# Optimization experiments

Hardware: AMD Instinct MI355X
Metric: run time of the kernel (lower is better)

The kernel has to match this reference:

```python
import jax, jax.numpy as jnp
import numpy as np

NB, NT, P = 20000, 1000, 50000
MARGIN = 2.0
LAM = 0.5          # lambda_param
TOPK = 5
RANK_W = 0.3
NEG_SENT = -1e9    # sentinel for masked-out (positive-labeled) entries


def setup_inputs() -> dict:
    key = jax.random.key(0)
    k1, k2, k3 = jax.random.split(key, 3)
    scores = jax.random.normal(k1, (NB, NT), dtype=jnp.float32)
    pair_bacteria = jax.random.randint(k2, (P,), 0, NB)
    pair_traits = jax.random.randint(k3, (P,), 0, NT)
    return {"scores": scores, "pair_bacteria": pair_bacteria, "pair_traits": pair_traits}


def reference(scores, pair_bacteria, pair_traits):
    nb, nt = scores.shape
    # scatter labels: labels[b, t] = 1 for each positive pair
    labels = jnp.zeros_like(scores).at[pair_bacteria, pair_traits].set(1.0)

    # HCMGNN-style weighted squared-diff loss on sigmoid predictions
    preds = jax.nn.sigmoid(scores)
    diff = labels - preds
    total = float(nb * nt)
    sq = diff * diff
    positive_loss = jnp.sum(labels * sq) / total
    negative_loss = jnpp_sum = jnp.sum((1.0 - labels) * sq) / total
    loss = (1.0 - LAM) * positive_loss + LAM * negative_loss

    # per-positive-pair top-k margin ranking loss
    rows = scores[pair_bacteria]          # [P, NT]
    row_labels = labels[pair_bacteria]    # [P, NT]
    masked = jnp.where(row_labels == 0.0, rows, NEG_SENT)
    top_neg, _ = jax.lax.top_k(masked, TOPK)               # [P, TOPK]
    pos_score = scores[pair_bacteria, pair_traits]         # [P]
    # sentinel entries give margin - pos + NEG_SENT << 0 -> relu = 0, grad = 0
    contrib = jax.nn.relu(MARGIN - (pos_score[:, None] - top_neg))
    ranking_sum = jnp.sum(contrib)

    num_neg_row = jnp.sum(row_labels == 0.0, axis=1)       # negatives per pair's row
    valid = jnp.minimum(num_neg_row, TOPK)                 # min(5, len(neg_scores))
    num_ranking_pairs = jnp.sum(valid)

    ranking_loss = ranking_sum / jnp.maximum(num_ranking_pairs, 1).astype(scores.dtype)
    loss = jnp.where(num_ranking_pairs > 0, loss + RANK_W * ranking_loss, loss)
    return loss
```

## Files before the change

### kernel.cpp

```cpp
#include <hip/hip_runtime.h>
#include <cstdint>
#include <cstddef>

#define NB 20000
#define NT 1000
#define P_PAIRS 50000
#define MARGIN 2.0f
#define RANK_W 0.3f
#define NEG_SENT -1e9f

#define BLOCK 512
#define ROWS_PB 32
#define NBLOCKS (NB / ROWS_PB)
#define PB4 (P_PAIRS / 4)
#define PLIST_CAP 512
#define MROW_W 33


#define INSERT5(x)                                        \
    {                                                     \
        float _x = (x);                                   \
        float n0 = fmaxf(t0, _x), s0_ = fminf(t0, _x);    \
        float n1 = fmaxf(t1, s0_), s1_ = fminf(t1, s0_);  \
        float n2 = fmaxf(t2, s1_), s2_ = fminf(t2, s1_);  \
        float n3 = fmaxf(t3, s2_), s3_ = fminf(t3, s2_);  \
        float n4 = fmaxf(t4, s3_);                        \
        t0 = n0; t1 = n1; t2 = n2; t3 = n3; t4 = n4;      \
    }

#define PROC1(xv, lab)                                              \
    {                                                               \
        float _x = (xv);                                            \
        int _lab = (lab);                                           \
        float _s = __builtin_amdgcn_rcpf(1.0f + __expf(-_x));       \
        float _d = (float)_lab - _s;                                \
        sq = fmaf(_d, _d, sq);                                      \
        pcount += _lab;                                             \
        float _xx = _lab ? NEG_SENT : _x;                           \
        INSERT5(_xx);                                               \
    }

#define PROC4(v, bits)                        \
    PROC1((v).x, (int)(((bits) >> 0) & 1u));  \
    PROC1((v).y, (int)(((bits) >> 1) & 1u));  \
    PROC1((v).z, (int)(((bits) >> 2) & 1u));  \
    PROC1((v).w, (int)(((bits) >> 3) & 1u));

#define SCAN4(v, idx)                                                   \
    {                                                                   \
        int _bs[4] = {(v).x, (v).y, (v).z, (v).w};                      \
        _Pragma("unroll")                                               \
        for (int _j = 0; _j < 4; ++_j) {                                \
            unsigned int _d = (unsigned int)(_bs[_j] - rowBase);        \
            if (_d < (unsigned int)ROWS_PB) {                           \
                int _t = pt[(idx) * 4 + _j];                            \
                atomicOr(&smask[_d * MROW_W + (_t >> 5)], 1u << (_t & 31)); \
                int _k = atomicAdd(&pcnt, 1);                           \
                if (_k < PLIST_CAP) plist[_k] = ((int)_d << 10) | _t;   \
            }                                                           \
        }                                                               \
    }

__global__ __launch_bounds__(BLOCK)
void fused_row_pair_kernel(const float* __restrict__ scores,
                           const int* __restrict__ pb,
                           const int* __restrict__ pt,
                           float4* __restrict__ partials) {
    const int tid  = threadIdx.x;
    const int lane = tid & 63;
    const int wib  = tid >> 6;
    const int grp  = lane >> 4;
    const int gl   = lane & 15;
    const int rowBase = blockIdx.x * ROWS_PB;

    __shared__ unsigned int smask[ROWS_PB * MROW_W];
    __shared__ float  stop5[ROWS_PB][5];
    __shared__ int    snn[ROWS_PB];
    __shared__ int    plist[PLIST_CAP];
    __shared__ int    pcnt;
    __shared__ float  bsq[ROWS_PB];
    __shared__ float  sc[8];
    __shared__ unsigned int sv[8];

    for (int i = tid; i < ROWS_PB * MROW_W; i += BLOCK) smask[i] = 0u;
    if (tid == 0) pcnt = 0;
    __syncthreads();

    const int4* pb4 = reinterpret_cast<const int4*>(pb);
    #pragma unroll 1
    for (int base = tid; base + 1536 < PB4; base += 2048) {
        int4 va = pb4[base       ];
        int4 vb = pb4[base +  512];
        int4 vc = pb4[base + 1024];
        int4 vd = pb4[base + 1536];
        SCAN4(va, base);
        SCAN4(vb, base +  512);
        SCAN4(vc, base + 1024);
        SCAN4(vd, base + 1536);
    }
    {
        int idx = 12288 + tid;
        if (idx < PB4) {
            int4 v = pb4[idx];
            SCAN4(v, idx);
        }
    }
    __syncthreads();

    const int localRow = wib * 4 + grp;
    const int row = rowBase + localRow;
    const float4* rowp = reinterpret_cast<const float4*>(scores + (size_t)row * NT);
    const unsigned int* mrow = smask + localRow * MROW_W;
    const int wb = gl >> 3;
    const int sh = (gl & 7) * 4;

    float t0 = NEG_SENT, t1 = NEG_SENT, t2 = NEG_SENT, t3 = NEG_SENT, t4 = NEG_SENT;
    float sq = 0.0f;
    int pcount = 0;

    {
        float4 v0  = rowp[gl      ];
        float4 v1  = rowp[gl +  16];
        float4 v2  = rowp[gl +  32];
        float4 v3  = rowp[gl +  48];
        unsigned int b0 = (mrow[wb     ] >> sh) & 0xFu;
        unsigned int b1 = (mrow[wb +  2] >> sh) & 0xFu;
        unsigned int b2 = (mrow[wb +  4] >> sh) & 0xFu;
        unsigned int b3 = (mrow[wb +  6] >> sh) & 0xFu;
        PROC4(v0, b0); PROC4(v1, b1); PROC4(v2, b2); PROC4(v3, b3);
    }
    {
        float4 v0  = rowp[gl +  64];
        float4 v1  = rowp[gl +  80];
        float4 v2  = rowp[gl +  96];
        float4 v3  = rowp[gl + 112];
        unsigned int b0 = (mrow[wb +  8] >> sh) & 0xFu;
        unsigned int b1 = (mrow[wb + 10] >> sh) & 0xFu;
        unsigned int b2 = (mrow[wb + 12] >> sh) & 0xFu;
        unsigned int b3 = (mrow[wb + 14] >> sh) & 0xFu;
        PROC4(v0, b0); PROC4(v1, b1); PROC4(v2, b2); PROC4(v3, b3);
    }
    {
        float4 v0  = rowp[gl + 128];
        float4 v1  = rowp[gl + 144];
        float4 v2  = rowp[gl + 160];
        float4 v3  = rowp[gl + 176];
        unsigned int b0 = (mrow[wb + 16] >> sh) & 0xFu;
        unsigned int b1 = (mrow[wb + 18] >> sh) & 0xFu;
        unsigned int b2 = (mrow[wb + 20] >> sh) & 0xFu;
        unsigned int b3 = (mrow[wb + 22] >> sh) & 0xFu;
        PROC4(v0, b0); PROC4(v1, b1); PROC4(v2, b2); PROC4(v3, b3);
    }
    {
        float4 v0  = rowp[gl + 192];
        float4 v1  = rowp[gl + 208];
        float4 v2  = rowp[gl + 224];
        unsigned int b0 = (mrow[wb + 24] >> sh) & 0xFu;
        unsigned int b1 = (mrow[wb + 26] >> sh) & 0xFu;
        unsigned int b2 = (mrow[wb + 28] >> sh) & 0xFu;
        PROC4(v0, b0); PROC4(v1, b1); PROC4(v2, b2);
    }
    if (gl < 10) {
        float4 v = rowp[gl + 240];
        unsigned int bt = (mrow[wb + 30] >> sh) & 0xFu;
        PROC4(v, bt);
    }

    #pragma unroll
    for (int off = 8; off >= 1; off >>= 1) {
        float b0 = __shfl_xor(t0, off, 16);
        float b1 = __shfl_xor(t1, off, 16);
        float b2 = __shfl_xor(t2, off, 16);
        float b3 = __shfl_xor(t3, off, 16);
        float b4 = __shfl_xor(t4, off, 16);
        sq     += __shfl_xor(sq, off, 16);
        pcount += __shfl_xor(pcount, off, 16);

        float m1  = fminf(t0, b0);
        float m2a = fminf(t1, b0), m2b = fminf(t0, b1);
        float m3a = fminf(t2, b0), m3b = fminf(t1, b1), m3c = fminf(t0, b2);
        float m4a = fminf(t3, b0), m4b = fminf(t2, b1), m4c = fminf(t1, b2), m4d = fminf(t0, b3);
        float c0 = fmaxf(t0, b0);
        float c1 = fmaxf(fmaxf(t1, b1), m1);
        float c2 = fmaxf(fmaxf(t2, b2), fmaxf(m2a, m2b));
        float c3 = fmaxf(fmaxf(t3, b3), fmaxf(fmaxf(m3a, m3b), m3c));
        float c4 = fmaxf(fmaxf(t4, b4), fmaxf(fmaxf(m4a, m4b), fmaxf(m4c, m4d)));
        t0 = c0; t1 = c1; t2 = c2; t3 = c3; t4 = c4;
    }

    if (gl == 0) {
        stop5[localRow][0] = t0; stop5[localRow][1] = t1; stop5[localRow][2] = t2;
        stop5[localRow][3] = t3; stop5[localRow][4] = t4;
        snn[localRow] = NT - pcount;
        bsq[localRow] = sq;
    }
    __syncthreads();

    float c = 0.0f;
    unsigned int valid = 0;
    int np = pcnt;
    if (np <= PLIST_CAP) {
        for (int k = tid; k < np; k += BLOCK) {
            int e = plist[k];
            int lr = e >> 10, t = e & 1023;
            float pos = scores[(size_t)(rowBase + lr) * NT + t];
            #pragma unroll
            for (int q = 0; q < 5; ++q) {
                float contrib = MARGIN - (pos - stop5[lr][q]);
                c += contrib > 0.0f ? contrib : 0.0f;
            }
            int nn = snn[lr];
            valid += (unsigned int)(nn < 5 ? nn : 5);
        }
    } else {
        for (int i = tid; i < PB4; i += BLOCK) {
            int4 v = pb4[i];
            int bs[4] = {v.x, v.y, v.z, v.w};
            #pragma unroll
            for (int j = 0; j < 4; ++j) {
                unsigned int d = (unsigned int)(bs[j] - rowBase);
                if (d < (unsigned int)ROWS_PB) {
                    int t = pt[i * 4 + j];
                    float pos = scores[(size_t)(rowBase + d) * NT + t];
                    #pragma unroll
                    for (int q = 0; q < 5; ++q) {
                        float contrib = MARGIN - (pos - stop5[d][q]);
                        c += contrib > 0.0f ? contrib : 0.0f;
                    }
                    int nn = snn[d];
                    valid += (unsigned int)(nn < 5 ? nn : 5);
                }
            }
        }
    }

    #pragma unroll
    for (int off = 32; off >= 1; off >>= 1) {
        c     += __shfl_xor(c, off);
        valid += __shfl_xor(valid, off);
    }
    if ((tid & 63) == 0) { sc[wib] = c; sv[wib] = valid; }
    __syncthreads();
    if (tid == 0) {
        float s = 0.0f;
        #pragma unroll
        for (int k = 0; k < ROWS_PB; ++k) s += bsq[k];
        float cb = 0.0f;
        float vb = 0.0f;
        #pragma unroll
        for (int w = 0; w < 8; ++w) { cb += sc[w]; vb += (float)sv[w]; }
        partials[blockIdx.x] = make_float4(s, cb, vb, 0.0f);
    }
}

__global__ __launch_bounds__(256)
void finalize_kernel(const float4* __restrict__ partials,
                     float* __restrict__ out) {
    float s = 0.0f, cb = 0.0f, vb = 0.0f;
    for (int i = threadIdx.x; i < NBLOCKS; i += 256) {
        float4 p = partials[i];
        s += p.x; cb += p.y; vb += p.z;
    }
    #pragma unroll
    for (int off = 32; off >= 1; off >>= 1) {
        s  += __shfl_xor(s, off);
        cb += __shfl_xor(cb, off);
        vb += __shfl_xor(vb, off);
    }
    __shared__ float ss[4], scc[4], svv[4];
    int wib = threadIdx.x >> 6;
    if ((threadIdx.x & 63) == 0) { ss[wib] = s; scc[wib] = cb; svv[wib] = vb; }
    __syncthreads();
    if (threadIdx.x == 0) {
        float st = ss[0] + ss[1] + ss[2] + ss[3];
        float ct = scc[0] + scc[1] + scc[2] + scc[3];
        float vt = svv[0] + svv[1] + svv[2] + svv[3];
        float loss = 0.5f * st / 2.0e7f;
        if (vt > 0.0f) loss += RANK_W * ct / vt;
        out[0] = loss;
    }
}

extern "C" void kernel_launch(void* const* d_in, const int* in_sizes, int n_in,
                              void* d_out, int out_size, void* d_ws, size_t ws_size,
                              hipStream_t stream) {
    const float* scores = (const float*)d_in[0];
    const int*   pb     = (const int*)d_in[1];
    const int*   pt     = (const int*)d_in[2];
    float*       out    = (float*)d_out;
    float4*      partials = (float4*)d_ws;

    fused_row_pair_kernel<<<NBLOCKS, BLOCK, 0, stream>>>(scores, pb, pt, partials);
    finalize_kernel<<<1, 256, 0, stream>>>(partials, out);
}
```

Measured before the change: 35.65 us.

## Pre-bucket pairs by row block in a scatter kernel instead of per-block full scans

Adds a scatter kernel that buckets positive pairs by 16-row block in global workspace, so each row block reads only its own pairs rather than scanning all pair indices. Rows per block and block size are halved. The final reduction kernel is replaced by global atomics plus a last-block ticket. This adds a zeroing kernel and a scatter kernel launch, and makes the floating-point summation order nondeterministic.

```diff
diff --git a/kernel.cpp b/kernel.cpp
--- a/kernel.cpp
+++ b/kernel.cpp
@@ -9,13 +9,32 @@
 #define RANK_W 0.3f
 #define NEG_SENT -1e9f
 
-#define BLOCK 512
-#define ROWS_PB 32
+#define BLOCK 256
+#define ROWS_PB 16
 #define NBLOCKS (NB / ROWS_PB)
 #define PB4 (P_PAIRS / 4)
-#define PLIST_CAP 512
+#define BUCKET_CAP 256
 #define MROW_W 33
 
+
+__global__ void zero_ctrl_kernel(unsigned int* __restrict__ ws) {
+    int i = blockIdx.x * blockDim.x + threadIdx.x;
+    if (i < 1254) ws[i] = 0u;
+}
+
+__global__ __launch_bounds__(256)
+void scatter_kernel(const int* __restrict__ pb,
+                    const int* __restrict__ pt,
+                    int* __restrict__ counts,
+                    int* __restrict__ lists) {
+    int p = blockIdx.x * 256 + threadIdx.x;
+    if (p >= P_PAIRS) return;
+    int b = pb[p];
+    int t = pt[p];
+    int blk = b >> 4;
+    int idx = atomicAdd(&counts[blk], 1);
+    if (idx < BUCKET_CAP) lists[blk * BUCKET_CAP + idx] = ((b & 15) << 10) | t;
+}
 
 #define INSERT5(x)                                        \
     {                                                     \
@@ -46,26 +65,17 @@
     PROC1((v).z, (int)(((bits) >> 2) & 1u));  \
     PROC1((v).w, (int)(((bits) >> 3) & 1u));
 
-#define SCAN4(v, idx)                                                   \
-    {                                                                   \
-        int _bs[4] = {(v).x, (v).y, (v).z, (v).w};                      \
-        _Pragma("unroll")                                               \
-        for (int _j = 0; _j < 4; ++_j) {                                \
-            unsigned int _d = (unsigned int)(_bs[_j] - rowBase);        \
-            if (_d < (unsigned int)ROWS_PB) {                           \
-                int _t = pt[(idx) * 4 + _j];                            \
-                atomicOr(&smask[_d * MROW_W + (_t >> 5)], 1u << (_t & 31)); \
-                int _k = atomicAdd(&pcnt, 1);                           \
-                if (_k < PLIST_CAP) plist[_k] = ((int)_d << 10) | _t;   \
-            }                                                           \
-        }                                                               \
-    }
-
 __global__ __launch_bounds__(BLOCK)
 void fused_row_pair_kernel(const float* __restrict__ scores,
                            const int* __restrict__ pb,
                            const int* __restrict__ pt,
-                           float4* __restrict__ partials) {
+                           const int* __restrict__ counts,
+                           const int* __restrict__ lists,
+                           float* __restrict__ sq_total,
+                           float* __restrict__ rsum,
+                           unsigned int* __restrict__ nrp,
+                           unsigned int* __restrict__ ticket,
+                           float* __restrict__ out) {
     const int tid  = threadIdx.x;
     const int lane = tid & 63;
     const int wib  = tid >> 6;
@@ -76,33 +86,36 @@
     __shared__ unsigned int smask[ROWS_PB * MROW_W];
     __shared__ float  stop5[ROWS_PB][5];
     __shared__ int    snn[ROWS_PB];
-    __shared__ int    plist[PLIST_CAP];
-    __shared__ int    pcnt;
+    __shared__ int    plist[BUCKET_CAP];
     __shared__ float  bsq[ROWS_PB];
-    __shared__ float  sc[8];
-    __shared__ unsigned int sv[8];
+    __shared__ float  sc[4];
+    __shared__ unsigned int sv[4];
 
     for (int i = tid; i < ROWS_PB * MROW_W; i += BLOCK) smask[i] = 0u;
-    if (tid == 0) pcnt = 0;
-    __syncthreads();
-
-    const int4* pb4 = reinterpret_cast<const int4*>(pb);
-    #pragma unroll 1
-    for (int base = tid; base + 1536 < PB4; base += 2048) {
-        int4 va = pb4[base       ];
-        int4 vb = pb4[base +  512];
-        int4 vc = pb4[base + 1024];
-        int4 vd = pb4[base + 1536];
-        SCAN4(va, base);
-        SCAN4(vb, base +  512);
-        SCAN4(vc, base + 1024);
-        SCAN4(vd, base + 1536);
-    }
-    {
-        int idx = 12288 + tid;
-        if (idx < PB4) {
-            int4 v = pb4[idx];
-            SCAN4(v, idx);
+    __syncthreads();
+
+    const int rawCnt = counts[blockIdx.x];
+    const bool overflow = rawCnt > BUCKET_CAP;
+    const int cnt = overflow ? 0 : rawCnt;
+    if (tid < cnt) {
+        int e = lists[blockIdx.x * BUCKET_CAP + tid];
+        plist[tid] = e;
+        int lr = e >> 10, t = e & 1023;
+        atomicOr(&smask[lr * MROW_W + (t >> 5)], 1u << (t & 31));
+    }
+    if (overflow) {
+        const int4* pb4 = reinterpret_cast<const int4*>(pb);
+        for (int i = tid; i < PB4; i += BLOCK) {
+            int4 v = pb4[i];
+            int bs[4] = {v.x, v.y, v.z, v.w};
+            #pragma unroll
+            for (int j = 0; j < 4; ++j) {
+                unsigned int d = (unsigned int)(bs[j] - rowBase);
+                if (d < (unsigned int)ROWS_PB) {
+                    int t = pt[i * 4 + j];
+                    atomicOr(&smask[d * MROW_W + (t >> 5)], 1u << (t & 31));
+                }
+            }
         }
     }
     __syncthreads();
@@ -119,10 +132,10 @@
     int pcount = 0;
 
     {
-        float4 v0  = rowp[gl      ];
-        float4 v1  = rowp[gl +  16];
-        float4 v2  = rowp[gl +  32];
-        float4 v3  = rowp[gl +  48];
+        float4 v0 = rowp[gl      ];
+        float4 v1 = rowp[gl +  16];
+        float4 v2 = rowp[gl +  32];
+        float4 v3 = rowp[gl +  48];
         unsigned int b0 = (mrow[wb     ] >> sh) & 0xFu;
         unsigned int b1 = (mrow[wb +  2] >> sh) & 0xFu;
         unsigned int b2 = (mrow[wb +  4] >> sh) & 0xFu;
@@ -130,10 +143,10 @@
         PROC4(v0, b0); PROC4(v1, b1); PROC4(v2, b2); PROC4(v3, b3);
     }
     {
-        float4 v0  = rowp[gl +  64];
-        float4 v1  = rowp[gl +  80];
-        float4 v2  = rowp[gl +  96];
-        float4 v3  = rowp[gl + 112];
+        float4 v0 = rowp[gl +  64];
+        float4 v1 = rowp[gl +  80];
+        float4 v2 = rowp[gl +  96];
+        float4 v3 = rowp[gl + 112];
         unsigned int b0 = (mrow[wb +  8] >> sh) & 0xFu;
         unsigned int b1 = (mrow[wb + 10] >> sh) & 0xFu;
         unsigned int b2 = (mrow[wb + 12] >> sh) & 0xFu;
@@ -141,10 +154,10 @@
         PROC4(v0, b0); PROC4(v1, b1); PROC4(v2, b2); PROC4(v3, b3);
     }
     {
-        float4 v0  = rowp[gl + 128];
-        float4 v1  = rowp[gl + 144];
-        float4 v2  = rowp[gl + 160];
-        float4 v3  = rowp[gl + 176];
+        float4 v0 = rowp[gl + 128];
+        float4 v1 = rowp[gl + 144];
+        float4 v2 = rowp[gl + 160];
+        float4 v3 = rowp[gl + 176];
         unsigned int b0 = (mrow[wb + 16] >> sh) & 0xFu;
         unsigned int b1 = (mrow[wb + 18] >> sh) & 0xFu;
         unsigned int b2 = (mrow[wb + 20] >> sh) & 0xFu;
@@ -152,9 +165,9 @@
         PROC4(v0, b0); PROC4(v1, b1); PROC4(v2, b2); PROC4(v3, b3);
     }
     {
-        float4 v0  = rowp[gl + 192];
-        float4 v1  = rowp[gl + 208];
-        float4 v2  = rowp[gl + 224];
+        float4 v0 = rowp[gl + 192];
+        float4 v1 = rowp[gl + 208];
+        float4 v2 = rowp[gl + 224];
         unsigned int b0 = (mrow[wb + 24] >> sh) & 0xFu;
         unsigned int b1 = (mrow[wb + 26] >> sh) & 0xFu;
         unsigned int b2 = (mrow[wb + 28] >> sh) & 0xFu;
@@ -198,9 +211,8 @@
 
     float c = 0.0f;
     unsigned int valid = 0;
-    int np = pcnt;
-    if (np <= PLIST_CAP) {
-        for (int k = tid; k < np; k += BLOCK) {
+    if (!overflow) {
+        for (int k = tid; k < cnt; k += BLOCK) {
             int e = plist[k];
             int lr = e >> 10, t = e & 1023;
             float pos = scores[(size_t)(rowBase + lr) * NT + t];
@@ -213,6 +225,7 @@
             valid += (unsigned int)(nn < 5 ? nn : 5);
         }
     } else {
+        const int4* pb4 = reinterpret_cast<const int4*>(pb);
         for (int i = tid; i < PB4; i += BLOCK) {
             int4 v = pb4[i];
             int bs[4] = {v.x, v.y, v.z, v.w};
@@ -241,43 +254,24 @@
     }
     if ((tid & 63) == 0) { sc[wib] = c; sv[wib] = valid; }
     __syncthreads();
+
     if (tid == 0) {
         float s = 0.0f;
         #pragma unroll
         for (int k = 0; k < ROWS_PB; ++k) s += bsq[k];
-        float cb = 0.0f;
-        float vb = 0.0f;
-        #pragma unroll
-        for (int w = 0; w < 8; ++w) { cb += sc[w]; vb += (float)sv[w]; }
-        partials[blockIdx.x] = make_float4(s, cb, vb, 0.0f);
-    }
-}
-
-__global__ __launch_bounds__(256)
-void finalize_kernel(const float4* __restrict__ partials,
-                     float* __restrict__ out) {
-    float s = 0.0f, cb = 0.0f, vb = 0.0f;
-    for (int i = threadIdx.x; i < NBLOCKS; i += 256) {
-        float4 p = partials[i];
-        s += p.x; cb += p.y; vb += p.z;
-    }
-    #pragma unroll
-    for (int off = 32; off >= 1; off >>= 1) {
-        s  += __shfl_xor(s, off);
-        cb += __shfl_xor(cb, off);
-        vb += __shfl_xor(vb, off);
-    }
-    __shared__ float ss[4], scc[4], svv[4];
-    int wib = threadIdx.x >> 6;
-    if ((threadIdx.x & 63) == 0) { ss[wib] = s; scc[wib] = cb; svv[wib] = vb; }
-    __syncthreads();
-    if (threadIdx.x == 0) {
-        float st = ss[0] + ss[1] + ss[2] + ss[3];
-        float ct = scc[0] + scc[1] + scc[2] + scc[3];
-        float vt = svv[0] + svv[1] + svv[2] + svv[3];
-        float loss = 0.5f * st / 2.0e7f;
-        if (vt > 0.0f) loss += RANK_W * ct / vt;
-        out[0] = loss;
+        atomicAdd(sq_total, s);
+        atomicAdd(rsum, sc[0] + sc[1] + sc[2] + sc[3]);
+        atomicAdd(nrp,  sv[0] + sv[1] + sv[2] + sv[3]);
+        __threadfence();
+        unsigned int done = atomicAdd(ticket, 1u);
+        if (done == NBLOCKS - 1) {
+            float sqt = atomicAdd(sq_total, 0.0f);
+            float rs  = atomicAdd(rsum, 0.0f);
+            unsigned int n = atomicAdd(nrp, 0u);
+            float loss = 0.5f * sqt / 2.0e7f;
+            if (n > 0) loss += RANK_W * rs / (float)n;
+            out[0] = loss;
+        }
     }
 }
 
@@ -288,8 +282,17 @@
     const int*   pb     = (const int*)d_in[1];
     const int*   pt     = (const int*)d_in[2];
     float*       out    = (float*)d_out;
-    float4*      partials = (float4*)d_ws;
-
-    fused_row_pair_kernel<<<NBLOCKS, BLOCK, 0, stream>>>(scores, pb, pt, partials);
-    finalize_kernel<<<1, 256, 0, stream>>>(partials, out);
-}
+
+    char* ws = (char*)d_ws;
+    int*          counts   = (int*)ws;
+    float*        sq_total = (float*)(ws + 5000);
+    float*        rsum     = (float*)(ws + 5004);
+    unsigned int* nrp      = (unsigned int*)(ws + 5008);
+    unsigned int* ticket   = (unsigned int*)(ws + 5012);
+    int*          lists    = (int*)(ws + 5120);
+
+    zero_ctrl_kernel<<<5, 256, 0, stream>>>((unsigned int*)ws);
+    scatter_kernel<<<(P_PAIRS + 255) / 256, 256, 0, stream>>>(pb, pt, counts, lists);
+    fused_row_pair_kernel<<<NBLOCKS, BLOCK, 0, stream>>>(
+        scores, pb, pt, counts, lists, sq_total, rsum, nrp, ticket, out);
+}
```

Result: slower. 93.52 us (+162.3%).
